# Performance work log

Hardware: AMD Instinct MI355X
Metric: run time of the kernel (lower is better)

Reference implementation:

```python
import jax, jax.numpy as jnp
import numpy as np


def setup_inputs() -> dict:
    key = jax.random.key(0)
    k0, k1, k2, k3, k4 = jax.random.split(key, 5)
    B, S, D, E, H = 2, 4096, 1024, 8, 512
    x = jax.random.normal(k0, (B, S, D), jnp.float32)
    w_router = jax.random.normal(k1, (D, E), jnp.float32) * (D ** -0.5)
    w1 = jax.random.normal(k2, (E, D, H), jnp.float32) * (D ** -0.5)
    w2 = jax.random.normal(k3, (E, H, D), jnp.float32) * (H ** -0.5)
    w3 = jax.random.normal(k4, (E, D, H), jnp.float32) * (D ** -0.5)
    return {"x": x, "w_router": w_router, "w1": w1, "w2": w2, "w3": w3, "top_k": 2}


def reference(x, w_router, w1, w2, w3, top_k):
    """MoE layer: linear router -> softmax -> top_k, then grouped SwiGLU experts
    combined with the routing weights. out = sum_k w_k * Expert_{idx_k}(x)."""
    B, S, D = x.shape
    E = w_router.shape[1]
    xt = x.reshape(-1, D)                              # [T, D]
    T = xt.shape[0]

    # Router
    logits = xt @ w_router                             # [T, E]
    probs = jax.nn.softmax(logits, axis=-1)
    weights, idx = jax.lax.top_k(probs, top_k)         # [T, k], [T, k]

    # Scatter top-k weights into a dense per-token gate over experts.
    gate = jnp.zeros((T, E), xt.dtype).at[jnp.arange(T)[:, None], idx].add(weights)

    h = jax.nn.silu(jnp.einsum('td,edh->teh', xt, w1)) * jnp.einsum('td,edh->teh', xt, w3)
    y = jnp.einsum('te,teh,ehd->td', gate, h, w2)      # combine
    return y.reshape(B, S, D)
```

## Files before the change

### kernel.cpp

```cpp
#include <hip/hip_runtime.h>

#define NT    8192
#define DIM   1024
#define NE    8
#define NH    512
#define NROWS (NT*2)

typedef _Float16 f16;
typedef unsigned int u32;
typedef __attribute__((ext_vector_type(8))) _Float16 f16x8;
typedef __attribute__((ext_vector_type(4))) _Float16 f16x4;
typedef __attribute__((ext_vector_type(2))) _Float16 f16x2;
typedef __attribute__((ext_vector_type(4))) float f32x4;

__device__ __forceinline__ void gl2lds16(const f16* gptr, f16* ldsptr) {
    __builtin_amdgcn_global_load_lds(
        (const __attribute__((address_space(1))) u32*)gptr,
        (__attribute__((address_space(3))) u32*)ldsptr, 16, 0, 0);
}

#define FR(sbuf, row, q) \
    (*(const f16x8*)&sbuf[(row)*32 + (((q) ^ (((row) >> 1) & 3)) << 3)])

#define KC 512
__global__ __launch_bounds__(256) void prep_kernel(
    const float* __restrict__ x, const float* __restrict__ wr,
    const float* __restrict__ w1, const float* __restrict__ w3,
    const float* __restrict__ w2, float* __restrict__ plogits,
    f16* __restrict__ w1t, f16* __restrict__ w3t, f16* __restrict__ w2t)
{
    __shared__ float smem[NE*KC];
    int tid = threadIdx.x;
    int bi = blockIdx.x;
    if (bi < 1024) {
        int bx = bi & 511, by = bi >> 9;
        int kc0 = by * KC;
        for (int i = tid; i < NE*KC; i += 256) {
            int k = i >> 3, e = i & 7;
            smem[e*KC + k] = wr[(size_t)kc0*NE + i];
        }
        __syncthreads();
        int tok = bx*16 + (tid >> 4);
        int kl  = tid & 15;
        float acc[NE];
        #pragma unroll
        for (int e = 0; e < NE; e++) acc[e] = 0.f;
        const float* xrow = x + (size_t)tok*DIM + kc0;
        #pragma unroll
        for (int i = 0; i < KC/64; i++) {
            int kb = i*64 + kl*4;
            float4 xv = *(const float4*)(xrow + kb);
            #pragma unroll
            for (int e = 0; e < NE; e++) {
                float4 wv = *(const float4*)&smem[e*KC + kb];
                acc[e] += xv.x*wv.x + xv.y*wv.y + xv.z*wv.z + xv.w*wv.w;
            }
        }
        #pragma unroll
        for (int e = 0; e < NE; e++) {
            float v = acc[e];
            v += __shfl_xor(v, 1); v += __shfl_xor(v, 2);
            v += __shfl_xor(v, 4); v += __shfl_xor(v, 8);
            acc[e] = v;
        }
        if (kl == 0) {
            float* pp = plogits + ((size_t)by*NT + tok)*NE;
            float4 o0 = {acc[0], acc[1], acc[2], acc[3]};
            float4 o1 = {acc[4], acc[5], acc[6], acc[7]};
            *(float4*)pp = o0;
            *(float4*)(pp + 4) = o1;
        }
    } else {
        int tz = bi - 1024;
        int zx = tz & 511, zy = tz >> 9;
        int tensor = zy >> 3, e = zy & 7;
        const float* src; f16* dst; int R, C;
        if (tensor == 0)      { src = w1; dst = w1t; R = DIM; C = NH; }
        else if (tensor == 1) { src = w3; dst = w3t; R = DIM; C = NH; }
        else                  { src = w2; dst = w2t; R = NH; C = DIM; }
        src += (size_t)e * DIM * NH;
        dst += (size_t)e * DIM * NH;
        int tcols = C >> 5;
        int bx = zx % tcols, by = zx / tcols;
        int r0 = by*32, c0 = bx*32;
        int tx = tid & 31, ty = tid >> 5;
        #pragma unroll
        for (int i = ty; i < 32; i += 8)
            smem[i*33 + tx] = src[(size_t)(r0+i)*C + c0 + tx];
        __syncthreads();
        int p = tid & 15;
        #pragma unroll
        for (int pass = 0; pass < 2; pass++) {
            int i = (tid >> 4) + pass*16;
            f16x2 v = { (f16)smem[(2*p)*33 + i], (f16)smem[(2*p+1)*33 + i] };
            *(f16x2*)&dst[(size_t)(c0+i)*R + r0 + 2*p] = v;
        }
    }
}

__global__ __launch_bounds__(1024) void finalize_kernel(
    const float* __restrict__ plogits, int* __restrict__ tok_ids,
    int* __restrict__ aid, float* __restrict__ row_gate, int* __restrict__ offs)
{
    __shared__ unsigned char s_e[NROWS];
    __shared__ float s_w[NROWS];
    __shared__ int hist[NE], cur[NE];
    int tid = threadIdx.x;
    if (tid < NE) hist[tid] = 0;
    __syncthreads();

    #pragma unroll 1
    for (int it = 0; it < NT/1024; it++) {
        int t = it*1024 + tid;
        const float* p0 = plogits + (size_t)t*NE;
        const float* p1 = plogits + (size_t)NT*NE + (size_t)t*NE;
        float4 a0 = *(const float4*)p0, a1 = *(const float4*)(p0+4);
        float4 b0 = *(const float4*)p1, b1 = *(const float4*)(p1+4);
        float l[NE] = { a0.x+b0.x, a0.y+b0.y, a0.z+b0.z, a0.w+b0.w,
                        a1.x+b1.x, a1.y+b1.y, a1.z+b1.z, a1.w+b1.w };
        float m = l[0];
        #pragma unroll
        for (int e = 1; e < NE; e++) m = fmaxf(m, l[e]);
        float s = 0.f;
        #pragma unroll
        for (int e = 0; e < NE; e++) { l[e] = __expf(l[e] - m); s += l[e]; }
        float inv = 1.f / s;
        int i0 = 0; float v0 = l[0];
        #pragma unroll
        for (int e = 1; e < NE; e++) if (l[e] > v0) { v0 = l[e]; i0 = e; }
        int i1 = -1; float v1 = -1.f;
        #pragma unroll
        for (int e = 0; e < NE; e++) if (e != i0 && l[e] > v1) { v1 = l[e]; i1 = e; }
        s_e[t*2+0] = (unsigned char)i0; s_w[t*2+0] = v0*inv;
        s_e[t*2+1] = (unsigned char)i1; s_w[t*2+1] = v1*inv;
        #pragma unroll
        for (int ee = 0; ee < NE; ee++) {
            int c = __popcll(__ballot(i0 == ee)) + __popcll(__ballot(i1 == ee));
            if ((tid & 63) == 0 && c) atomicAdd(&hist[ee], c);
        }
    }
    __syncthreads();

    if (tid == 0) {
        int s = 0;
        #pragma unroll
        for (int e = 0; e < NE; e++) { offs[e] = s; cur[e] = s; s += hist[e]; }
        offs[NE] = s;
    }
    __syncthreads();

    unsigned long long ltmask = (1ULL << (tid & 63)) - 1;
    #pragma unroll 1
    for (int it = 0; it < NROWS/1024; it++) {
        int id = it*1024 + tid;
        int e = s_e[id];
        int pos = 0;
        #pragma unroll
        for (int ee = 0; ee < NE; ee++) {
            unsigned long long mk = __ballot(e == ee);
            int cnt = __popcll(mk);
            int b = 0;
            if ((tid & 63) == 0 && cnt) b = atomicAdd(&cur[ee], cnt);
            b = __shfl(b, 0);
            if (e == ee) pos = b + __popcll(mk & ltmask);
        }
        tok_ids[pos] = id >> 1;
        aid[pos] = id;
        row_gate[pos] = s_w[id];
    }
}

#define BK 64

#define BM1 64
#define BN1 128
__global__ __launch_bounds__(256,3) void gemm1_kernel(
    const float* __restrict__ x, const int* __restrict__ tok_ids,
    const f16* __restrict__ w1t, const f16* __restrict__ w3t,
    f16* __restrict__ gbuf, const int* __restrict__ offs)
{
    int bi = blockIdx.x;
    int e  = bi & 7;
    int r_ = bi >> 3;
    int nt = r_ & 3;
    int mt = r_ >> 2;
    int off = offs[e];
    int n_e = offs[e+1] - off;
    if (mt*BM1 >= n_e) return;

    __shared__ f16 sA [2][BM1*32];
    __shared__ f16 sB1[2][BN1*32];
    __shared__ f16 sB3[2][BN1*32];
    __shared__ int stok[BM1];

    int tid = threadIdx.x;
    if (tid < BM1) {
        int rloc = mt*BM1 + tid; rloc = rloc < n_e ? rloc : n_e - 1;
        stok[tid] = tok_ids[off + rloc];
    }
    __syncthreads();

    int lane = tid & 63, w = tid >> 6;
    int wcol = w*32;
    int q = lane >> 4, lm = lane & 15;

    int rA = tid >> 2, gA = tid & 3;
    const float* xr = x + (size_t)stok[rA]*DIM + gA*8;
    int pA = (gA ^ ((rA>>1)&3)) << 3;
    f16* sA0p = &sA[0][rA*32 + pA];
    f16* sA1p = &sA[1][rA*32 + pA];

    int lr0 = w*32 + (lane >> 2);
    int lr1 = lr0 + 16;
    int g0 = (lane & 3) ^ ((lr0 >> 1) & 3);
    int g1 = (lane & 3) ^ ((lr1 >> 1) & 3);
    const f16* w1p = w1t + ((size_t)e*NH + nt*BN1)*DIM;
    const f16* w3p = w3t + ((size_t)e*NH + nt*BN1)*DIM;
    const f16* pB1_0 = w1p + (size_t)lr0*DIM + g0*8;
    const f16* pB1_1 = w1p + (size_t)lr1*DIM + g1*8;
    const f16* pB3_0 = w3p + (size_t)lr0*DIM + g0*8;
    const f16* pB3_1 = w3p + (size_t)lr1*DIM + g1*8;
    int lofs0 = lr0*32 + ((lane & 3) << 3);
    int lofs1 = lr1*32 + ((lane & 3) << 3);

    f32x4 acc1[4][2], acc3[4][2];
    #pragma unroll
    for (int a = 0; a < 4; a++)
        #pragma unroll
        for (int b = 0; b < 2; b++) {
            acc1[a][b] = (f32x4){0.f,0.f,0.f,0.f};
            acc3[a][b] = (f32x4){0.f,0.f,0.f,0.f};
        }

    float4 a00 = *(const float4*)(xr);
    float4 a01 = *(const float4*)(xr + 4);
    float4 a10 = *(const float4*)(xr + 32);
    float4 a11 = *(const float4*)(xr + 36);

    for (int k0 = 0; k0 < DIM; k0 += BK) {
        __syncthreads();
        *(f16x8*)sA0p = (f16x8){ (f16)a00.x,(f16)a00.y,(f16)a00.z,(f16)a00.w,
                                 (f16)a01.x,(f16)a01.y,(f16)a01.z,(f16)a01.w };
        *(f16x8*)sA1p = (f16x8){ (f16)a10.x,(f16)a10.y,(f16)a10.z,(f16)a10.w,
                                 (f16)a11.x,(f16)a11.y,(f16)a11.z,(f16)a11.w };
        gl2lds16(pB1_0 + k0,      &sB1[0][lofs0]);
        gl2lds16(pB1_1 + k0,      &sB1[0][lofs1]);
        gl2lds16(pB1_0 + k0 + 32, &sB1[1][lofs0]);
        gl2lds16(pB1_1 + k0 + 32, &sB1[1][lofs1]);
        gl2lds16(pB3_0 + k0,      &sB3[0][lofs0]);
        gl2lds16(pB3_1 + k0,      &sB3[0][lofs1]);
        gl2lds16(pB3_0 + k0 + 32, &sB3[1][lofs0]);
        gl2lds16(pB3_1 + k0 + 32, &sB3[1][lofs1]);
        __syncthreads();
        if (k0 + BK < DIM) {
            a00 = *(const float4*)(xr + k0 + BK);
            a01 = *(const float4*)(xr + k0 + BK + 4);
            a10 = *(const float4*)(xr + k0 + BK + 32);
            a11 = *(const float4*)(xr + k0 + BK + 36);
        }
        #pragma unroll
        for (int ks = 0; ks < 2; ks++) {
            f16x8 aF[4], b1F[2], b3F[2];
            #pragma unroll
            for (int s = 0; s < 4; s++) aF[s] = FR(sA[ks], s*16 + lm, q);
            #pragma unroll
            for (int c = 0; c < 2; c++) {
                b1F[c] = FR(sB1[ks], wcol + c*16 + lm, q);
                b3F[c] = FR(sB3[ks], wcol + c*16 + lm, q);
            }
            #pragma unroll
            for (int sr = 0; sr < 4; sr++)
                #pragma unroll
                for (int sc = 0; sc < 2; sc++) {
                    acc1[sr][sc] = __builtin_amdgcn_mfma_f32_16x16x32_f16(aF[sr], b1F[sc], acc1[sr][sc], 0, 0, 0);
                    acc3[sr][sc] = __builtin_amdgcn_mfma_f32_16x16x32_f16(aF[sr], b3F[sc], acc3[sr][sc], 0, 0, 0);
                }
        }
    }
    #pragma unroll
    for (int sr = 0; sr < 4; sr++) {
        #pragma unroll
        for (int reg = 0; reg < 4; reg++) {
            int row = mt*BM1 + sr*16 + q*4 + reg;
            if (row < n_e) {
                #pragma unroll
                for (int sc = 0; sc < 2; sc++) {
                    int col = nt*BN1 + wcol + sc*16 + lm;
                    float h1 = acc1[sr][sc][reg];
                    float h3 = acc3[sr][sc][reg];
                    float gv = h1 / (1.f + __expf(-h1)) * h3;
                    gbuf[(size_t)(off + row)*NH + col] = (f16)gv;
                }
            }
        }
    }
}

#define BM 128
#define BN 128
__global__ __launch_bounds__(256,3) void gemm2_kernel(
    const f16* __restrict__ gbuf, const f16* __restrict__ w2t,
    const int* __restrict__ offs, const int* __restrict__ aid,
    const float* __restrict__ row_gate, f16* __restrict__ ybuf)
{
    int bi = blockIdx.x;
    int e  = bi & 7;
    int r_ = bi >> 3;
    int nt = r_ & 7;
    int mt = r_ >> 3;
    int off = offs[e];
    int n_e = offs[e+1] - off;
    if (mt*BM >= n_e) return;

    __shared__ f16 sA[2][BM*32];
    __shared__ f16 sB[2][BN*32];
    __shared__ int said[BM];
    __shared__ float sgate[BM];

    int tid = threadIdx.x;
    if (tid < BM) {
        int rloc = mt*BM + tid;
        if (rloc < n_e) { said[tid] = aid[off + rloc]; sgate[tid] = row_gate[off + rloc]; }
        else            { said[tid] = 0; sgate[tid] = 0.f; }
    }

    int lane = tid & 63, w = tid >> 6;
    int wrow = (w >> 1)*64, wcol = (w & 1)*64;
    int q = lane >> 4, lm = lane & 15;

    int lr0 = w*32 + (lane >> 2);
    int lr1 = lr0 + 16;
    int g0 = (lane & 3) ^ ((lr0 >> 1) & 3);
    int g1 = (lane & 3) ^ ((lr1 >> 1) & 3);
    int ga0 = mt*BM + lr0; ga0 = ga0 < n_e ? ga0 : n_e - 1;
    int ga1 = mt*BM + lr1; ga1 = ga1 < n_e ? ga1 : n_e - 1;
    const f16* pA0 = gbuf + (size_t)(off + ga0)*NH + g0*8;
    const f16* pA1 = gbuf + (size_t)(off + ga1)*NH + g1*8;
    const f16* w2p = w2t + ((size_t)e*DIM + nt*BN)*NH;
    const f16* pB0 = w2p + (size_t)lr0*NH + g0*8;
    const f16* pB1 = w2p + (size_t)lr1*NH + g1*8;
    int lofs0 = lr0*32 + ((lane & 3) << 3);
    int lofs1 = lr1*32 + ((lane & 3) << 3);

    f32x4 acc[4][4];
    #pragma unroll
    for (int a = 0; a < 4; a++)
        #pragma unroll
        for (int b = 0; b < 4; b++) acc[a][b] = (f32x4){0.f,0.f,0.f,0.f};

    __syncthreads();

    for (int k0 = 0; k0 < NH; k0 += BK) {
        gl2lds16(pA0 + k0,      &sA[0][lofs0]);
        gl2lds16(pA1 + k0,      &sA[0][lofs1]);
        gl2lds16(pA0 + k0 + 32, &sA[1][lofs0]);
        gl2lds16(pA1 + k0 + 32, &sA[1][lofs1]);
        gl2lds16(pB0 + k0,      &sB[0][lofs0]);
        gl2lds16(pB1 + k0,      &sB[0][lofs1]);
        gl2lds16(pB0 + k0 + 32, &sB[1][lofs0]);
        gl2lds16(pB1 + k0 + 32, &sB[1][lofs1]);
        __syncthreads();
        #pragma unroll
        for (int ks = 0; ks < 2; ks++) {
            f16x8 aF[4], bF[4];
            #pragma unroll
            for (int s = 0; s < 4; s++) {
                aF[s] = FR(sA[ks], wrow + s*16 + lm, q);
                bF[s] = FR(sB[ks], wcol + s*16 + lm, q);
            }
            #pragma unroll
            for (int sr = 0; sr < 4; sr++)
                #pragma unroll
                for (int sc = 0; sc < 4; sc++)
                    acc[sr][sc] = __builtin_amdgcn_mfma_f32_16x16x32_f16(aF[sr], bF[sc], acc[sr][sc], 0, 0, 0);
        }
        __syncthreads();
    }
    #pragma unroll
    for (int sr = 0; sr < 4; sr++) {
        #pragma unroll
        for (int reg = 0; reg < 4; reg++) {
            int lrow = wrow + sr*16 + q*4 + reg;
            if (mt*BM + lrow < n_e) {
                int id = said[lrow];
                float wgt = sgate[lrow];
                #pragma unroll
                for (int sc = 0; sc < 4; sc++) {
                    int col = nt*BN + wcol + sc*16 + lm;
                    ybuf[(size_t)id*DIM + col] = (f16)(wgt * acc[sr][sc][reg]);
                }
            }
        }
    }
}

__global__ __launch_bounds__(256) void combine_kernel(
    const f16* __restrict__ ybuf, float* __restrict__ out)
{
    int gid = blockIdx.x*256 + threadIdx.x;
    int t = gid >> 7;
    int c = (gid & 127) << 3;
    f16x8 y0 = *(const f16x8*)(ybuf + ((size_t)2*t)*DIM + c);
    f16x8 y1 = *(const f16x8*)(ybuf + ((size_t)2*t+1)*DIM + c);
    float* op = out + (size_t)t*DIM + c;
    float4 o0 = { (float)y0[0] + (float)y1[0], (float)y0[1] + (float)y1[1],
                  (float)y0[2] + (float)y1[2], (float)y0[3] + (float)y1[3] };
    float4 o1 = { (float)y0[4] + (float)y1[4], (float)y0[5] + (float)y1[5],
                  (float)y0[6] + (float)y1[6], (float)y0[7] + (float)y1[7] };
    *(float4*)op = o0;
    *(float4*)(op + 4) = o1;
}

extern "C" void kernel_launch(void* const* d_in, const int* in_sizes, int n_in,
                              void* d_out, int out_size, void* d_ws, size_t ws_size,
                              hipStream_t stream)
{
    const float* x  = (const float*)d_in[0];
    const float* wr = (const float*)d_in[1];
    const float* w1 = (const float*)d_in[2];
    const float* w2 = (const float*)d_in[3];
    const float* w3 = (const float*)d_in[4];
    float* out = (float*)d_out;

    char* ws = (char*)d_ws;
    f16* ybuf    = (f16*)ws;        ws += (size_t)NROWS*DIM*sizeof(f16);
    f16* w1t     = (f16*)ws;        ws += (size_t)NE*NH*DIM*sizeof(f16);
    f16* w3t     = (f16*)ws;        ws += (size_t)NE*NH*DIM*sizeof(f16);
    f16* w2t     = (f16*)ws;        ws += (size_t)NE*DIM*NH*sizeof(f16);
    f16* gbuf    = (f16*)ws;        ws += (size_t)NROWS*NH*sizeof(f16);
    float* plogits = (float*)ws;    ws += (size_t)2*NT*NE*4;
    int* tok_ids = (int*)ws;        ws += (size_t)NROWS*4;
    int* aid     = (int*)ws;        ws += (size_t)NROWS*4;
    float* row_gate = (float*)ws;   ws += (size_t)NROWS*4;
    int* offs    = (int*)ws;        ws += 64;
    if (ws_size < (size_t)(ws - (char*)d_ws)) return;

    prep_kernel<<<1024 + 12288, 256, 0, stream>>>(x, wr, w1, w3, w2,
                                                  plogits, w1t, w3t, w2t);
    finalize_kernel<<<1, 1024, 0, stream>>>(plogits, tok_ids, aid, row_gate, offs);
    gemm1_kernel<<<8192, 256, 0, stream>>>(x, tok_ids, w1t, w3t, gbuf, offs);
    gemm2_kernel<<<8192, 256, 0, stream>>>(gbuf, w2t, offs, aid, row_gate, ybuf);
    combine_kernel<<<(NT*(DIM/8))/256, 256, 0, stream>>>(ybuf, out);
}
```

Measured before the change: 271.4 us.

## Enlarge gemm1 tile to 128x128 and deepen gemm2 K-step to 128

gemm1 now uses a 128-row by 128-column tile with a 2x2 wave layout. Each wave computes 64x64 outputs for both the w1 and w3 products, and each thread loads 32 contiguous fp32 x values per K-step. This doubles reuse of the weight tiles and halves the grid, at the cost of more accumulator registers (occupancy bound lowered to 2). gemm2 loads 128 K-elements per barrier into four LDS slices, halving the number of barriers but doubling LDS use, with launch bounds also lowered to 2.

New measurement: 302.1 us. 1.11x slower.

```diff
diff --git a/kernel.cpp b/kernel.cpp
--- a/kernel.cpp
+++ b/kernel.cpp
@@ -170,11 +170,10 @@
     }
 }
 
-#define BK 64
-
-#define BM1 64
+
+#define BM1 128
 #define BN1 128
-__global__ __launch_bounds__(256,3) void gemm1_kernel(
+__global__ __launch_bounds__(256,2) void gemm1_kernel(
     const float* __restrict__ x, const int* __restrict__ tok_ids,
     const f16* __restrict__ w1t, const f16* __restrict__ w3t,
     f16* __restrict__ gbuf, const int* __restrict__ offs)
@@ -201,14 +200,13 @@
     __syncthreads();
 
     int lane = tid & 63, w = tid >> 6;
-    int wcol = w*32;
+    int wrow = (w >> 1)*64, wcol = (w & 1)*64;
     int q = lane >> 4, lm = lane & 15;
 
-    int rA = tid >> 2, gA = tid & 3;
-    const float* xr = x + (size_t)stok[rA]*DIM + gA*8;
-    int pA = (gA ^ ((rA>>1)&3)) << 3;
-    f16* sA0p = &sA[0][rA*32 + pA];
-    f16* sA1p = &sA[1][rA*32 + pA];
+    int rA = tid >> 1, h = tid & 1;
+    const float* xr = x + (size_t)stok[rA]*DIM + h*32;
+    int swz = (rA >> 1) & 3;
+    f16* sAp = &sA[h][rA*32];
 
     int lr0 = w*32 + (lane >> 2);
     int lr1 = lr0 + 16;
@@ -223,26 +221,28 @@
     int lofs0 = lr0*32 + ((lane & 3) << 3);
     int lofs1 = lr1*32 + ((lane & 3) << 3);
 
-    f32x4 acc1[4][2], acc3[4][2];
+    f32x4 acc1[4][4], acc3[4][4];
     #pragma unroll
     for (int a = 0; a < 4; a++)
         #pragma unroll
-        for (int b = 0; b < 2; b++) {
+        for (int b = 0; b < 4; b++) {
             acc1[a][b] = (f32x4){0.f,0.f,0.f,0.f};
             acc3[a][b] = (f32x4){0.f,0.f,0.f,0.f};
         }
 
-    float4 a00 = *(const float4*)(xr);
-    float4 a01 = *(const float4*)(xr + 4);
-    float4 a10 = *(const float4*)(xr + 32);
-    float4 a11 = *(const float4*)(xr + 36);
-
-    for (int k0 = 0; k0 < DIM; k0 += BK) {
-        __syncthreads();
-        *(f16x8*)sA0p = (f16x8){ (f16)a00.x,(f16)a00.y,(f16)a00.z,(f16)a00.w,
-                                 (f16)a01.x,(f16)a01.y,(f16)a01.z,(f16)a01.w };
-        *(f16x8*)sA1p = (f16x8){ (f16)a10.x,(f16)a10.y,(f16)a10.z,(f16)a10.w,
-                                 (f16)a11.x,(f16)a11.y,(f16)a11.z,(f16)a11.w };
+    float4 ax[8];
+    #pragma unroll
+    for (int i = 0; i < 8; i++) ax[i] = *(const float4*)(xr + i*4);
+
+    for (int k0 = 0; k0 < DIM; k0 += 64) {
+        __syncthreads();
+        #pragma unroll
+        for (int g = 0; g < 4; g++) {
+            float4 lo = ax[2*g], hi = ax[2*g+1];
+            *(f16x8*)&sAp[((g ^ swz) << 3)] =
+                (f16x8){ (f16)lo.x,(f16)lo.y,(f16)lo.z,(f16)lo.w,
+                         (f16)hi.x,(f16)hi.y,(f16)hi.z,(f16)hi.w };
+        }
         gl2lds16(pB1_0 + k0,      &sB1[0][lofs0]);
         gl2lds16(pB1_1 + k0,      &sB1[0][lofs1]);
         gl2lds16(pB1_0 + k0 + 32, &sB1[1][lofs0]);
@@ -252,26 +252,24 @@
         gl2lds16(pB3_0 + k0 + 32, &sB3[1][lofs0]);
         gl2lds16(pB3_1 + k0 + 32, &sB3[1][lofs1]);
         __syncthreads();
-        if (k0 + BK < DIM) {
-            a00 = *(const float4*)(xr + k0 + BK);
-            a01 = *(const float4*)(xr + k0 + BK + 4);
-            a10 = *(const float4*)(xr + k0 + BK + 32);
-            a11 = *(const float4*)(xr + k0 + BK + 36);
+        if (k0 + 64 < DIM) {
+            #pragma unroll
+            for (int i = 0; i < 8; i++)
+                ax[i] = *(const float4*)(xr + k0 + 64 + i*4);
         }
         #pragma unroll
         for (int ks = 0; ks < 2; ks++) {
-            f16x8 aF[4], b1F[2], b3F[2];
-            #pragma unroll
-            for (int s = 0; s < 4; s++) aF[s] = FR(sA[ks], s*16 + lm, q);
-            #pragma unroll
-            for (int c = 0; c < 2; c++) {
-                b1F[c] = FR(sB1[ks], wcol + c*16 + lm, q);
-                b3F[c] = FR(sB3[ks], wcol + c*16 + lm, q);
+            f16x8 aF[4], b1F[4], b3F[4];
+            #pragma unroll
+            for (int s = 0; s < 4; s++) {
+                aF[s]  = FR(sA[ks],  wrow + s*16 + lm, q);
+                b1F[s] = FR(sB1[ks], wcol + s*16 + lm, q);
+                b3F[s] = FR(sB3[ks], wcol + s*16 + lm, q);
             }
             #pragma unroll
             for (int sr = 0; sr < 4; sr++)
                 #pragma unroll
-                for (int sc = 0; sc < 2; sc++) {
+                for (int sc = 0; sc < 4; sc++) {
                     acc1[sr][sc] = __builtin_amdgcn_mfma_f32_16x16x32_f16(aF[sr], b1F[sc], acc1[sr][sc], 0, 0, 0);
                     acc3[sr][sc] = __builtin_amdgcn_mfma_f32_16x16x32_f16(aF[sr], b3F[sc], acc3[sr][sc], 0, 0, 0);
                 }
@@ -281,10 +279,10 @@
     for (int sr = 0; sr < 4; sr++) {
         #pragma unroll
         for (int reg = 0; reg < 4; reg++) {
-            int row = mt*BM1 + sr*16 + q*4 + reg;
+            int row = mt*BM1 + wrow + sr*16 + q*4 + reg;
             if (row < n_e) {
                 #pragma unroll
-                for (int sc = 0; sc < 2; sc++) {
+                for (int sc = 0; sc < 4; sc++) {
                     int col = nt*BN1 + wcol + sc*16 + lm;
                     float h1 = acc1[sr][sc][reg];
                     float h3 = acc3[sr][sc][reg];
@@ -298,7 +296,7 @@
 
 #define BM 128
 #define BN 128
-__global__ __launch_bounds__(256,3) void gemm2_kernel(
+__global__ __launch_bounds__(256,2) void gemm2_kernel(
     const f16* __restrict__ gbuf, const f16* __restrict__ w2t,
     const int* __restrict__ offs, const int* __restrict__ aid,
     const float* __restrict__ row_gate, f16* __restrict__ ybuf)
@@ -312,8 +310,8 @@
     int n_e = offs[e+1] - off;
     if (mt*BM >= n_e) return;
 
-    __shared__ f16 sA[2][BM*32];
-    __shared__ f16 sB[2][BN*32];
+    __shared__ f16 sA[4][BM*32];
+    __shared__ f16 sB[4][BN*32];
     __shared__ int said[BM];
     __shared__ float sgate[BM];
 
@@ -350,18 +348,17 @@
 
     __syncthreads();
 
-    for (int k0 = 0; k0 < NH; k0 += BK) {
-        gl2lds16(pA0 + k0,      &sA[0][lofs0]);
-        gl2lds16(pA1 + k0,      &sA[0][lofs1]);
-        gl2lds16(pA0 + k0 + 32, &sA[1][lofs0]);
-        gl2lds16(pA1 + k0 + 32, &sA[1][lofs1]);
-        gl2lds16(pB0 + k0,      &sB[0][lofs0]);
-        gl2lds16(pB1 + k0,      &sB[0][lofs1]);
-        gl2lds16(pB0 + k0 + 32, &sB[1][lofs0]);
-        gl2lds16(pB1 + k0 + 32, &sB[1][lofs1]);
-        __syncthreads();
-        #pragma unroll
-        for (int ks = 0; ks < 2; ks++) {
+    for (int k0 = 0; k0 < NH; k0 += 128) {
+        #pragma unroll
+        for (int s = 0; s < 4; s++) {
+            gl2lds16(pA0 + k0 + s*32, &sA[s][lofs0]);
+            gl2lds16(pA1 + k0 + s*32, &sA[s][lofs1]);
+            gl2lds16(pB0 + k0 + s*32, &sB[s][lofs0]);
+            gl2lds16(pB1 + k0 + s*32, &sB[s][lofs1]);
+        }
+        __syncthreads();
+        #pragma unroll
+        for (int ks = 0; ks < 4; ks++) {
             f16x8 aF[4], bF[4];
             #pragma unroll
             for (int s = 0; s < 4; s++) {
@@ -438,7 +435,7 @@
     prep_kernel<<<1024 + 12288, 256, 0, stream>>>(x, wr, w1, w3, w2,
                                                   plogits, w1t, w3t, w2t);
     finalize_kernel<<<1, 1024, 0, stream>>>(plogits, tok_ids, aid, row_gate, offs);
-    gemm1_kernel<<<8192, 256, 0, stream>>>(x, tok_ids, w1t, w3t, gbuf, offs);
+    gemm1_kernel<<<4096, 256, 0, stream>>>(x, tok_ids, w1t, w3t, gbuf, offs);
     gemm2_kernel<<<8192, 256, 0, stream>>>(gbuf, w2t, offs, aid, row_gate, ybuf);
     combine_kernel<<<(NT*(DIM/8))/256, 256, 0, stream>>>(ybuf, out);
 }
```
